# Optimization experiments

Measured on AMD Instinct MI355X. Metric: run time of the kernel, lower is better.

Reference implementation:

```python
import jax, jax.numpy as jnp
import numpy as np

N_NODES = 100000
H = 256
E = 500000

def setup_inputs() -> dict:
    key = jax.random.key(0)
    ks = jax.random.split(key, 7)
    z_src = jax.random.normal(ks[0], (N_NODES, H), dtype=jnp.float32)
    z_dst = jax.random.normal(ks[1], (N_NODES, H), dtype=jnp.float32)
    edge_label_index = jax.random.randint(ks[2], (2, E), 0, N_NODES, dtype=jnp.int64)
    # Linear params, scaled like torch default init (~1/sqrt(fan_in))
    w1 = jax.random.normal(ks[3], (H, 2 * H), dtype=jnp.float32) * (1.0 / np.sqrt(2 * H))
    b1 = jax.random.normal(ks[4], (H,), dtype=jnp.float32) * (1.0 / np.sqrt(2 * H))
    w2 = jax.random.normal(ks[5], (1, H), dtype=jnp.float32) * (1.0 / np.sqrt(H))
    b2 = jax.random.normal(ks[6], (1,), dtype=jnp.float32) * (1.0 / np.sqrt(H))
    return {"z_src": z_src, "z_dst": z_dst, "edge_label_index": edge_label_index,
            "w1": w1, "b1": b1, "w2": w2, "b2": b2}

def reference(z_src, z_dst, edge_label_index, w1, b1, w2, b2):
    row, col = edge_label_index[0], edge_label_index[1]
    # gather edge endpoint features and concat -> [E, 2H]
    z = jnp.concatenate([z_src[row], z_dst[col]], axis=-1)
    z = jax.nn.relu(jnp.einsum('eh,oh->eo', z, w1) + b1)  # [E, H]
    z = jnp.einsum('eh,oh->eo', z, w2) + b2               # [E, 1]
    return jax.nn.sigmoid(z).reshape(-1)
```

## Files before the change

kernel.cpp:

```cpp
#include <hip/hip_runtime.h>

#define E_TOT 500000
#define N_NODES 100000
#define RB 128
#define NBH2 ((N_NODES + RB - 1) / RB)
#define CSTR 264

typedef __attribute__((ext_vector_type(8))) short short8;
typedef __attribute__((ext_vector_type(4))) float f32x4;

__device__ __forceinline__ unsigned short f2bf(float f) {
  union { float f; unsigned u; } x; x.f = f;
  unsigned r = x.u + 0x7fffu + ((x.u >> 16) & 1u);
  return (unsigned short)(r >> 16);
}

__device__ __forceinline__ float bf2f(unsigned short s) {
  union { unsigned u; float f; } x; x.u = ((unsigned)s) << 16;
  return x.f;
}

__device__ __forceinline__ void gl_lds16(const void* g, void* l) {
  __builtin_amdgcn_global_load_lds(
      (const __attribute__((address_space(1))) void*)g,
      (__attribute__((address_space(3))) void*)l, 16, 0, 0);
}

__global__ void k_repack_w1h(const float* __restrict__ w1,
                             unsigned short* __restrict__ w1r2) {
  int o = blockIdx.x * 256 + threadIdx.x;
  int half = o >> 16;
  int kb = (o >> 11) & 31;
  int n = (o >> 3) & 255;
  int j = o & 7;
  w1r2[o] = f2bf(w1[n * 512 + half * 256 + kb * 8 + j]);
}

__global__ __launch_bounds__(512, 4) void k_node_gemm(
    const float* __restrict__ zsrc, const float* __restrict__ zdst,
    const unsigned short* __restrict__ w1r2, const float* __restrict__ b1,
    unsigned short* __restrict__ Uo, unsigned short* __restrict__ Vo) {
  __shared__ __align__(16) char smem[RB * CSTR * 2];
  unsigned short* A_lds = (unsigned short*)smem;
  unsigned short* B_lds = (unsigned short*)(smem + 16384);
  unsigned short* C_lds = (unsigned short*)smem;

  const int bi = blockIdx.x;
  const int half = (bi >= NBH2) ? 1 : 0;
  const int n0 = (bi - half * NBH2) * RB;
  const float* Z = half ? zdst : zsrc;
  unsigned short* O = half ? Vo : Uo;

  const unsigned tid = threadIdx.x;
  const unsigned l = tid & 63u;
  const unsigned w = tid >> 6;
  const unsigned l15 = l & 15u;
  const unsigned lg = l >> 4;

  const unsigned arow = tid >> 3;
  const unsigned kbl = tid & 7u;

  const float* aptr0;
  const float* aptr1;
  {
    int r0 = n0 + (int)arow;
    int r1 = n0 + (int)arow + 64;
    if (r0 > N_NODES - 1) r0 = N_NODES - 1;
    if (r1 > N_NODES - 1) r1 = N_NODES - 1;
    aptr0 = Z + (long)r0 * 256 + kbl * 8;
    aptr1 = Z + (long)r1 * 256 + kbl * 8;
  }

  f32x4 acc[8][2];
#pragma unroll
  for (int mf = 0; mf < 8; ++mf)
#pragma unroll
    for (int nf = 0; nf < 2; ++nf) acc[mf][nf] = (f32x4){0.f, 0.f, 0.f, 0.f};

  f32x4 fa00 = ((const f32x4*)aptr0)[0];
  f32x4 fa01 = ((const f32x4*)aptr0)[1];
  f32x4 fa10 = ((const f32x4*)aptr1)[0];
  f32x4 fa11 = ((const f32x4*)aptr1)[1];

  for (int c = 0; c < 4; ++c) {
    __syncthreads();

    short8 sa;
    sa[0] = (short)f2bf(fa00.x); sa[1] = (short)f2bf(fa00.y);
    sa[2] = (short)f2bf(fa00.z); sa[3] = (short)f2bf(fa00.w);
    sa[4] = (short)f2bf(fa01.x); sa[5] = (short)f2bf(fa01.y);
    sa[6] = (short)f2bf(fa01.z); sa[7] = (short)f2bf(fa01.w);
    *(short8*)&A_lds[(kbl * 128u + arow) * 8u] = sa;
    sa[0] = (short)f2bf(fa10.x); sa[1] = (short)f2bf(fa10.y);
    sa[2] = (short)f2bf(fa10.z); sa[3] = (short)f2bf(fa10.w);
    sa[4] = (short)f2bf(fa11.x); sa[5] = (short)f2bf(fa11.y);
    sa[6] = (short)f2bf(fa11.z); sa[7] = (short)f2bf(fa11.w);
    *(short8*)&A_lds[(kbl * 128u + arow + 64u) * 8u] = sa;

    const unsigned short* bsrc = w1r2 + half * 65536 + c * 16384;
#pragma unroll
    for (int q = 0; q < 4; ++q) {
      unsigned off = (w * 4u + (unsigned)q) * 512u;
      gl_lds16(bsrc + off + l * 8u, B_lds + off);
    }

    __syncthreads();

    if (c < 3) {
      const float* g0 = aptr0 + (c + 1) * 64;
      const float* g1 = aptr1 + (c + 1) * 64;
      fa00 = ((const f32x4*)g0)[0];
      fa01 = ((const f32x4*)g0)[1];
      fa10 = ((const f32x4*)g1)[0];
      fa11 = ((const f32x4*)g1)[1];
    }

#pragma unroll
    for (int ks = 0; ks < 2; ++ks) {
      unsigned kb = (unsigned)ks * 4u + lg;
      short8 bfr0 = *(const short8*)&B_lds[(kb * 256u + w * 32u + l15) * 8u];
      short8 bfr1 = *(const short8*)&B_lds[(kb * 256u + w * 32u + 16u + l15) * 8u];
#pragma unroll
      for (int mf = 0; mf < 8; ++mf) {
        short8 afr = *(const short8*)&A_lds[(kb * 128u + mf * 16u + l15) * 8u];
        acc[mf][0] =
            __builtin_amdgcn_mfma_f32_16x16x32_bf16(afr, bfr0, acc[mf][0], 0, 0, 0);
        acc[mf][1] =
            __builtin_amdgcn_mfma_f32_16x16x32_bf16(afr, bfr1, acc[mf][1], 0, 0, 0);
      }
    }
  }

  float b1v[2];
#pragma unroll
  for (int nf = 0; nf < 2; ++nf)
    b1v[nf] = half ? 0.f : b1[w * 32u + nf * 16u + l15];

  __syncthreads();
#pragma unroll
  for (int mf = 0; mf < 8; ++mf) {
#pragma unroll
    for (int nf = 0; nf < 2; ++nf) {
#pragma unroll
      for (int r = 0; r < 4; ++r) {
        unsigned row = mf * 16u + lg * 4u + (unsigned)r;
        unsigned col = w * 32u + (unsigned)nf * 16u + l15;
        C_lds[row * CSTR + col] = f2bf(acc[mf][nf][r] + b1v[nf]);
      }
    }
  }
  __syncthreads();
#pragma unroll
  for (int k = 0; k < 8; ++k) {
    unsigned u = tid + (unsigned)k * 512u;
    unsigned row = u >> 5;
    unsigned cu = u & 31u;
    if (n0 + (int)row < N_NODES) {
      short8 vv = *(const short8*)&C_lds[row * CSTR + cu * 8u];
      *(short8*)(O + (long)(n0 + row) * 256 + cu * 8u) = vv;
    }
  }
}

#define EK_ITER 16
__global__ __launch_bounds__(256, 6) void k_edge(
    const unsigned short* __restrict__ U, const unsigned short* __restrict__ V,
    const int* __restrict__ eli, const float* __restrict__ w2,
    const float* __restrict__ b2, float* __restrict__ out) {
  const int tid = threadIdx.x;
  const int g = tid >> 4;
  const int j = tid & 15;
  float w2v[16];
#pragma unroll
  for (int q = 0; q < 8; ++q) {
    w2v[q] = w2[8 * j + q];
    w2v[8 + q] = w2[128 + 8 * j + q];
  }
  const float b2v = b2[0];
  const long base = (long)blockIdx.x * (16 * EK_ITER) + g;

#define CLAMP_E(k) \
  (((base + 16 * (k)) < E_TOT) ? (base + 16 * (k)) : (long)(E_TOT - 1))

  long eP = CLAMP_E(0);
  int rA = eli[eP], cA = eli[E_TOT + eP];
  long eQ = CLAMP_E(1);
  int rB = eli[eQ], cB = eli[E_TOT + eQ];
  short8 uA0 = *(const short8*)(U + (long)rA * 256 + 8 * j);
  short8 uA1 = *(const short8*)(U + (long)rA * 256 + 128 + 8 * j);
  short8 vA0 = *(const short8*)(V + (long)cA * 256 + 8 * j);
  short8 vA1 = *(const short8*)(V + (long)cA * 256 + 128 + 8 * j);
  short8 uB0, uB1, vB0, vB1;

#pragma unroll
  for (int it2 = 0; it2 < EK_ITER / 2; ++it2) {
    {
      long eN = CLAMP_E(2 * it2 + 2);
      int rN = eli[eN], cN = eli[E_TOT + eN];
      uB0 = *(const short8*)(U + (long)rB * 256 + 8 * j);
      uB1 = *(const short8*)(U + (long)rB * 256 + 128 + 8 * j);
      vB0 = *(const short8*)(V + (long)cB * 256 + 8 * j);
      vB1 = *(const short8*)(V + (long)cB * 256 + 128 + 8 * j);
      rB = rN; cB = cN;
      float p = 0.f;
#pragma unroll
      for (int q = 0; q < 8; ++q) {
        float a0 = bf2f((unsigned short)uA0[q]) + bf2f((unsigned short)vA0[q]);
        float a1 = bf2f((unsigned short)uA1[q]) + bf2f((unsigned short)vA1[q]);
        p = fmaf(fmaxf(a0, 0.f), w2v[q], p);
        p = fmaf(fmaxf(a1, 0.f), w2v[8 + q], p);
      }
      p += __shfl_xor(p, 1);
      p += __shfl_xor(p, 2);
      p += __shfl_xor(p, 4);
      p += __shfl_xor(p, 8);
      long e = base + 16 * (2 * it2);
      if (j == 0 && e < E_TOT) out[e] = 1.f / (1.f + __expf(-(p + b2v)));
    }
    {
      long eN = CLAMP_E(2 * it2 + 3);
      int rN = eli[eN], cN = eli[E_TOT + eN];
      uA0 = *(const short8*)(U + (long)rB * 256 + 8 * j);
      uA1 = *(const short8*)(U + (long)rB * 256 + 128 + 8 * j);
      vA0 = *(const short8*)(V + (long)cB * 256 + 8 * j);
      vA1 = *(const short8*)(V + (long)cB * 256 + 128 + 8 * j);
      rB = rN; cB = cN;
      float p = 0.f;
#pragma unroll
      for (int q = 0; q < 8; ++q) {
        float a0 = bf2f((unsigned short)uB0[q]) + bf2f((unsigned short)vB0[q]);
        float a1 = bf2f((unsigned short)uB1[q]) + bf2f((unsigned short)vB1[q]);
        p = fmaf(fmaxf(a0, 0.f), w2v[q], p);
        p = fmaf(fmaxf(a1, 0.f), w2v[8 + q], p);
      }
      p += __shfl_xor(p, 1);
      p += __shfl_xor(p, 2);
      p += __shfl_xor(p, 4);
      p += __shfl_xor(p, 8);
      long e = base + 16 * (2 * it2 + 1);
      if (j == 0 && e < E_TOT) out[e] = 1.f / (1.f + __expf(-(p + b2v)));
    }
  }
#undef CLAMP_E
}

extern "C" void kernel_launch(void* const* d_in, const int* in_sizes, int n_in,
                              void* d_out, int out_size, void* d_ws,
                              size_t ws_size, hipStream_t stream) {
  const float* zsrc = (const float*)d_in[0];
  const float* zdst = (const float*)d_in[1];
  const int* eli = (const int*)d_in[2];
  const float* w1 = (const float*)d_in[3];
  const float* b1 = (const float*)d_in[4];
  const float* w2 = (const float*)d_in[5];
  const float* b2 = (const float*)d_in[6];
  float* out = (float*)d_out;

  const size_t uv_bytes = (size_t)N_NODES * 256 * 2;
  unsigned short* U = (unsigned short*)d_ws;
  unsigned short* V = (unsigned short*)((char*)d_ws + uv_bytes);
  unsigned short* w1r2 = (unsigned short*)((char*)d_ws + 2 * uv_bytes);

  k_repack_w1h<<<512, 256, 0, stream>>>(w1, w1r2);
  k_node_gemm<<<2 * NBH2, 512, 0, stream>>>(zsrc, zdst, w1r2, b1, U, V);
  int nbe = (E_TOT + 16 * EK_ITER - 1) / (16 * EK_ITER);
  k_edge<<<nbe, 256, 0, stream>>>(U, V, eli, w2, b2, out);
}
```

Baseline: 152.3 us.

## Load W1 fragments into registers, stage full A tile with XOR-swizzled LDS

The node GEMM kernel now loads each wave's W1 fragments for all four K chunks directly into registers instead of streaming them through LDS. It also issues all A-row global loads up front and converts the whole 128x256 bf16 A tile into LDS in one pass, using an XOR swizzle on the row index. This replaces the per-chunk double-synchronized loop with a single barrier. The aim is fewer barriers, more memory parallelism and fewer LDS bank conflicts, at the cost of much higher register use (32 short8 B values plus 16 f32x4 A values), which may lower occupancy under launch_bounds(512,4).

```diff
diff --git a/kernel.cpp b/kernel.cpp
--- a/kernel.cpp
+++ b/kernel.cpp
@@ -18,12 +18,6 @@
 __device__ __forceinline__ float bf2f(unsigned short s) {
   union { unsigned u; float f; } x; x.u = ((unsigned)s) << 16;
   return x.f;
-}
-
-__device__ __forceinline__ void gl_lds16(const void* g, void* l) {
-  __builtin_amdgcn_global_load_lds(
-      (const __attribute__((address_space(1))) void*)g,
-      (__attribute__((address_space(3))) void*)l, 16, 0, 0);
 }
 
 __global__ void k_repack_w1h(const float* __restrict__ w1,
@@ -42,7 +36,6 @@
     unsigned short* __restrict__ Uo, unsigned short* __restrict__ Vo) {
   __shared__ __align__(16) char smem[RB * CSTR * 2];
   unsigned short* A_lds = (unsigned short*)smem;
-  unsigned short* B_lds = (unsigned short*)(smem + 16384);
   unsigned short* C_lds = (unsigned short*)smem;
 
   const int bi = blockIdx.x;
@@ -57,18 +50,35 @@
   const unsigned l15 = l & 15u;
   const unsigned lg = l >> 4;
 
-  const unsigned arow = tid >> 3;
+  const unsigned short* bbase = w1r2 + half * 65536u;
+  short8 breg[4][2][2];
+#pragma unroll
+  for (int c = 0; c < 4; ++c)
+#pragma unroll
+    for (int ks = 0; ks < 2; ++ks)
+#pragma unroll
+      for (int nf = 0; nf < 2; ++nf) {
+        unsigned kb2 = (unsigned)c * 8u + (unsigned)ks * 4u + lg;
+        unsigned col = w * 32u + (unsigned)nf * 16u + l15;
+        breg[c][ks][nf] = *(const short8*)(bbase + (kb2 * 256u + col) * 8u);
+      }
+
+  const unsigned ar = tid >> 3;
   const unsigned kbl = tid & 7u;
-
-  const float* aptr0;
-  const float* aptr1;
-  {
-    int r0 = n0 + (int)arow;
-    int r1 = n0 + (int)arow + 64;
-    if (r0 > N_NODES - 1) r0 = N_NODES - 1;
-    if (r1 > N_NODES - 1) r1 = N_NODES - 1;
-    aptr0 = Z + (long)r0 * 256 + kbl * 8;
-    aptr1 = Z + (long)r1 * 256 + kbl * 8;
+  int r0 = n0 + (int)ar;
+  int r1 = n0 + (int)ar + 64;
+  if (r0 > N_NODES - 1) r0 = N_NODES - 1;
+  if (r1 > N_NODES - 1) r1 = N_NODES - 1;
+  const float* p0 = Z + (long)r0 * 256 + kbl * 8u;
+  const float* p1 = Z + (long)r1 * 256 + kbl * 8u;
+
+  f32x4 ga[4][2][2];
+#pragma unroll
+  for (int c = 0; c < 4; ++c) {
+    ga[c][0][0] = ((const f32x4*)(p0 + c * 64))[0];
+    ga[c][0][1] = ((const f32x4*)(p0 + c * 64))[1];
+    ga[c][1][0] = ((const f32x4*)(p1 + c * 64))[0];
+    ga[c][1][1] = ((const f32x4*)(p1 + c * 64))[1];
   }
 
   f32x4 acc[8][2];
@@ -77,56 +87,37 @@
 #pragma unroll
     for (int nf = 0; nf < 2; ++nf) acc[mf][nf] = (f32x4){0.f, 0.f, 0.f, 0.f};
 
-  f32x4 fa00 = ((const f32x4*)aptr0)[0];
-  f32x4 fa01 = ((const f32x4*)aptr0)[1];
-  f32x4 fa10 = ((const f32x4*)aptr1)[0];
-  f32x4 fa11 = ((const f32x4*)aptr1)[1];
-
+#pragma unroll
   for (int c = 0; c < 4; ++c) {
-    __syncthreads();
-
-    short8 sa;
-    sa[0] = (short)f2bf(fa00.x); sa[1] = (short)f2bf(fa00.y);
-    sa[2] = (short)f2bf(fa00.z); sa[3] = (short)f2bf(fa00.w);
-    sa[4] = (short)f2bf(fa01.x); sa[5] = (short)f2bf(fa01.y);
-    sa[6] = (short)f2bf(fa01.z); sa[7] = (short)f2bf(fa01.w);
-    *(short8*)&A_lds[(kbl * 128u + arow) * 8u] = sa;
-    sa[0] = (short)f2bf(fa10.x); sa[1] = (short)f2bf(fa10.y);
-    sa[2] = (short)f2bf(fa10.z); sa[3] = (short)f2bf(fa10.w);
-    sa[4] = (short)f2bf(fa11.x); sa[5] = (short)f2bf(fa11.y);
-    sa[6] = (short)f2bf(fa11.z); sa[7] = (short)f2bf(fa11.w);
-    *(short8*)&A_lds[(kbl * 128u + arow + 64u) * 8u] = sa;
-
-    const unsigned short* bsrc = w1r2 + half * 65536 + c * 16384;
-#pragma unroll
-    for (int q = 0; q < 4; ++q) {
-      unsigned off = (w * 4u + (unsigned)q) * 512u;
-      gl_lds16(bsrc + off + l * 8u, B_lds + off);
-    }
-
-    __syncthreads();
-
-    if (c < 3) {
-      const float* g0 = aptr0 + (c + 1) * 64;
-      const float* g1 = aptr1 + (c + 1) * 64;
-      fa00 = ((const f32x4*)g0)[0];
-      fa01 = ((const f32x4*)g0)[1];
-      fa10 = ((const f32x4*)g1)[0];
-      fa11 = ((const f32x4*)g1)[1];
-    }
-
+    unsigned kb = (unsigned)c * 8u + kbl;
+#pragma unroll
+    for (int rs = 0; rs < 2; ++rs) {
+      unsigned row = ar + (unsigned)rs * 64u;
+      short8 sa;
+      sa[0] = (short)f2bf(ga[c][rs][0].x); sa[1] = (short)f2bf(ga[c][rs][0].y);
+      sa[2] = (short)f2bf(ga[c][rs][0].z); sa[3] = (short)f2bf(ga[c][rs][0].w);
+      sa[4] = (short)f2bf(ga[c][rs][1].x); sa[5] = (short)f2bf(ga[c][rs][1].y);
+      sa[6] = (short)f2bf(ga[c][rs][1].z); sa[7] = (short)f2bf(ga[c][rs][1].w);
+      *(short8*)&A_lds[kb * 1024u + ((row ^ kbl) * 8u)] = sa;
+    }
+  }
+
+  __syncthreads();
+
+#pragma unroll
+  for (int c = 0; c < 4; ++c) {
 #pragma unroll
     for (int ks = 0; ks < 2; ++ks) {
-      unsigned kb = (unsigned)ks * 4u + lg;
-      short8 bfr0 = *(const short8*)&B_lds[(kb * 256u + w * 32u + l15) * 8u];
-      short8 bfr1 = *(const short8*)&B_lds[(kb * 256u + w * 32u + 16u + l15) * 8u];
+      unsigned kb = (unsigned)c * 8u + (unsigned)ks * 4u + lg;
+      unsigned x = kb & 7u;
 #pragma unroll
       for (int mf = 0; mf < 8; ++mf) {
-        short8 afr = *(const short8*)&A_lds[(kb * 128u + mf * 16u + l15) * 8u];
-        acc[mf][0] =
-            __builtin_amdgcn_mfma_f32_16x16x32_bf16(afr, bfr0, acc[mf][0], 0, 0, 0);
-        acc[mf][1] =
-            __builtin_amdgcn_mfma_f32_16x16x32_bf16(afr, bfr1, acc[mf][1], 0, 0, 0);
+        short8 afr =
+            *(const short8*)&A_lds[kb * 1024u + (((mf * 16u + l15) ^ x) * 8u)];
+        acc[mf][0] = __builtin_amdgcn_mfma_f32_16x16x32_bf16(
+            afr, breg[c][ks][0], acc[mf][0], 0, 0, 0);
+        acc[mf][1] = __builtin_amdgcn_mfma_f32_16x16x32_bf16(
+            afr, breg[c][ks][1], acc[mf][1], 0, 0, 0);
       }
     }
   }
```

Result: slower. 182.2 us (+19.6%).
